# Optimization experiments

Measured on AMD Instinct MI355X. Metric: run time of the kernel, lower is better.

## Reference

```python
import jax, jax.numpy as jnp
import numpy as np
import math

N_HEAD = 16
N_LATENTS = 64
CHUNK = 128
ROPE_THETA = 10000.0


def _rope_cos_sin(T, D, theta):
    # D = head_dim; freqs over D/2 pairs
    inv = 1.0 / (theta ** (jnp.arange(0, D, 2, dtype=jnp.float32) / D))  # [D/2]
    ang = jnp.arange(T, dtype=jnp.float32)[:, None] * inv[None, :]       # [T, D/2]
    return jnp.cos(ang), jnp.sin(ang)


def _apply_rope(k, cos, sin):
    # k: [B, T, H, D]; pairs are consecutive (2i, 2i+1)
    B, T, H, D = k.shape
    kr = k.reshape(B, T, H, D // 2, 2)
    a, b = kr[..., 0], kr[..., 1]
    c = cos[None, :, None, :]
    s = sin[None, :, None, :]
    out = jnp.stack([a * c - b * s, a * s + b * c], axis=-1)
    return out.reshape(B, T, H, D).astype(k.dtype)


def setup_inputs() -> dict:
    key = jax.random.key(0)
    ks = jax.random.split(key, 6)
    B, T, C = 8, 4096, 1024
    H, L = N_HEAD, N_LATENTS
    D = C // H
    std_in = 1.0 / math.sqrt(C)
    return {
        "x": jax.random.normal(ks[0], (B, T, C), jnp.float32),
        "latent_queries": jax.random.normal(ks[1], (1, L, H, D), jnp.float32) * (1.0 / math.sqrt(D)),
        "W_k": jax.random.normal(ks[2], (C, C), jnp.float32) * std_in,
        "W_v": jax.random.normal(ks[3], (C, C), jnp.float32) * std_in,
        "W_g": jax.random.normal(ks[4], (H * L, C), jnp.float32) * std_in,
        "W_p": jax.random.normal(ks[5], (C, C), jnp.float32) * std_in,
    }


def reference(x, latent_queries, W_k, W_v, W_g, W_p):
    B, T, C = x.shape
    H, L, cs = N_HEAD, N_LATENTS, CHUNK
    D = C // H
    scale = 1.0 / math.sqrt(D)

    k = (x @ W_k.T).reshape(B, T, H, D)
    v = (x @ W_v.T).reshape(B, T, H, D)
    cos, sin = _rope_cos_sin(T, D, ROPE_THETA)
    k = _apply_rope(k, cos, sin)

    # softmax-gated latent mixing weights: [B, T, H, L]
    gates = jax.nn.softmax((x @ W_g.T).reshape(B, T, H, L) * scale, axis=-1)

    q = jnp.transpose(latent_queries, (0, 2, 1, 3))          # [1, H, L, D]
    nc = T // cs
    kc = jnp.transpose(k, (0, 2, 1, 3)).reshape(B, H, nc, cs, D)
    vc = jnp.transpose(v, (0, 2, 1, 3)).reshape(B, H, nc, cs, D)

    # per-chunk SDPA with torch is_causal semantics: top-left aligned
    # lower-triangular mask (latent row i attends chunk cols j <= i)
    scores = jnp.einsum('zhld,bhncd->bhnlc', q, kc) * scale   # [B,H,nc,L,cs]
    causal = jnp.arange(cs)[None, :] <= jnp.arange(L)[:, None]  # [L, cs]
    scores = jnp.where(causal[None, None, None], scores, -jnp.inf)
    probs = jax.nn.softmax(scores, axis=-1)
    # matmul with V per chunk, SUM over chunks (as in the torch loop)
    attn = jnp.einsum('bhnlc,bhncd->bhld', probs, vc)         # [B,H,L,D]

    # weighted combine: einsum('bhls,bhtl->bhts') then [B,T,C]
    weighted = jnp.einsum('bhld,bthl->bthd', attn, gates)
    out = weighted.reshape(B, T, C) @ W_p.T
    return out
```

## Files before the change

### kernel.cpp

```cpp
#include <hip/hip_runtime.h>
#include <hip/hip_bf16.h>

typedef unsigned short u16;
typedef __attribute__((ext_vector_type(8))) short bf16x8;
typedef __attribute__((ext_vector_type(4))) float f32x4;
typedef __attribute__((ext_vector_type(4))) unsigned short u16x4;

#define DEVI static __device__ __forceinline__

DEVI u16 f2bf(float f) {
    union { __hip_bfloat16 h; u16 u; } cv;
    cv.h = __float2bfloat16(f);
    return cv.u;
}
DEVI float bf2f(u16 u) {
    union { u16 u; __hip_bfloat16 h; } cv;
    cv.u = u;
    return __bfloat162float(cv.h);
}

DEVI void gload_lds16(const void* g, void* l) {
    __builtin_amdgcn_global_load_lds(
        (const __attribute__((address_space(1))) unsigned int*)g,
        (__attribute__((address_space(3))) unsigned int*)l, 16, 0, 0);
}

#define BAR asm volatile("s_barrier" ::: "memory")
#define VMW(N) asm volatile("s_waitcnt vmcnt(" #N ")" ::: "memory")

__global__ void k_cvt(const float* __restrict__ in, u16* __restrict__ out, int n4) {
    int i = blockIdx.x * blockDim.x + threadIdx.x;
    int stride = gridDim.x * blockDim.x;
    for (; i < n4; i += stride) {
        float4 v = ((const float4*)in)[i];
        u16x4 o;
        o.x = f2bf(v.x); o.y = f2bf(v.y); o.z = f2bf(v.z); o.w = f2bf(v.w);
        ((u16x4*)out)[i] = o;
    }
}

__global__ void k_rope(float2* __restrict__ tab) {
    int i = blockIdx.x * 256 + threadIdx.x;
    int t = i >> 5, j = i & 31;
    float inv = powf(10000.f, -(float)j / 32.f);
    float ang = (float)t * inv;
    float s, c;
    sincosf(ang, &s, &c);
    tab[i] = make_float2(c, s);
}

template<int MODE>
__global__ __launch_bounds__(512, 2) void k_gemm256(
    const u16* __restrict__ A, const u16* __restrict__ Bw,
    void* __restrict__ Cout, const float2* __restrict__ rope)
{
    extern __shared__ char lds[];
    const int tid = threadIdx.x;
    const int lane = tid & 63, wid = tid >> 6;
    const int wr = wid >> 2, wc = wid & 3;
    const int koff = (lane >> 4) * 16;

    const int GX = (MODE == 0) ? 8 : 4;
    const int kx = GX >> 1;
    int orig = blockIdx.x + blockIdx.y * GX;
    int xcd = orig & 7, i = orig >> 3;
    int bx = (xcd % kx) * 2 + (i & 1);
    int by = (xcd / kx) * 32 + (i >> 1);
    const int row0 = by * 256, col0 = bx * 256;

    auto stage = [&](int s) {
        const int t = s >> 2;
        const int isB = s & 1;
        const int kh = (s >> 1) & 1;
        char* base = lds + isB * 65536 + (t & 1) * 32768 + kh * 16384;
        const int kbase = t * 64 + kh * 32;
#pragma unroll
        for (int j = 0; j < 2; ++j) {
            int idx = j * 512 + tid;
            int r = idx >> 2;
            int kc = idx & 3;
            int grow;
            if (isB) {
                grow = col0 + r;
            } else {
                grow = row0 + r;
                if (MODE == 0)
                    grow = ((grow >> 11) << 12) | (((grow >> 6) & 31) << 7) | (grow & 63);
            }
            const u16* g = (isB ? Bw : A) + (size_t)grow * 1024 + kbase + kc * 8;
            gload_lds16(g, base + j * 8192 + wid * 1024);
        }
    };

    bf16x8 af[8];
    bf16x8 bq[2];
    f32x4 acc[8][4];
#pragma unroll
    for (int m = 0; m < 8; ++m)
#pragma unroll
        for (int n = 0; n < 4; ++n) acc[m][n] = f32x4{0.f, 0.f, 0.f, 0.f};

#define LDA(T, KH) do { \
    const char* ab_ = lds + ((T) & 1) * 32768 + (KH) * 16384; \
    _Pragma("unroll") \
    for (int mf = 0; mf < 8; ++mf) \
        af[mf] = *(const bf16x8*)(ab_ + (wr * 128 + mf * 16 + (lane & 15)) * 64 + koff); \
} while (0)

#define LDB(T, KH, NH) do { \
    const char* bb_ = lds + 65536 + ((T) & 1) * 32768 + (KH) * 16384; \
    bq[0] = *(const bf16x8*)(bb_ + (wc * 64 + ((NH) * 2)     * 16 + (lane & 15)) * 64 + koff); \
    bq[1] = *(const bf16x8*)(bb_ + (wc * 64 + ((NH) * 2 + 1) * 16 + (lane & 15)) * 64 + koff); \
} while (0)

#define MMA(NH) do { \
    __builtin_amdgcn_s_setprio(1); \
    _Pragma("unroll") \
    for (int mf = 0; mf < 8; ++mf) { \
        acc[mf][2 * (NH)]     = __builtin_amdgcn_mfma_f32_16x16x32_bf16(af[mf], bq[0], acc[mf][2 * (NH)], 0, 0, 0); \
        acc[mf][2 * (NH) + 1] = __builtin_amdgcn_mfma_f32_16x16x32_bf16(af[mf], bq[1], acc[mf][2 * (NH) + 1], 0, 0, 0); \
    } \
    __builtin_amdgcn_s_setprio(0); \
} while (0)

#pragma unroll 1
    for (int s = 0; s < 7; ++s) stage(s);
    VMW(10);
    BAR;

#pragma unroll 1
    for (int t = 0; t < 14; ++t) {
        LDA(t, 0); LDB(t, 0, 0);
        stage(4 * t + 7);
        BAR; MMA(0); BAR;
        LDB(t, 0, 1);
        stage(4 * t + 8);
        BAR; MMA(1); VMW(10); BAR;
        LDA(t, 1); LDB(t, 1, 0);
        stage(4 * t + 9);
        BAR; MMA(0); BAR;
        LDB(t, 1, 1);
        stage(4 * t + 10);
        BAR; MMA(1); VMW(10); BAR;
    }
    LDA(14, 0); LDB(14, 0, 0); stage(63); BAR; MMA(0); BAR;
    LDB(14, 0, 1);                         BAR; MMA(1); VMW(8); BAR;
    LDA(14, 1); LDB(14, 1, 0);             BAR; MMA(0); BAR;
    LDB(14, 1, 1);                         BAR; MMA(1); VMW(4); BAR;
    LDA(15, 0); LDB(15, 0, 0);             BAR; MMA(0); BAR;
    LDB(15, 0, 1);                         BAR; MMA(1); VMW(0); BAR;
    LDA(15, 1); LDB(15, 1, 0);             BAR; MMA(0); BAR;
    LDB(15, 1, 1);                         BAR; MMA(1);

#undef LDA
#undef LDB
#undef MMA

    const int rbase = row0 + wr * 128 + ((lane >> 4) << 2);
    const int cbase = col0 + wc * 64 + (lane & 15);
#pragma unroll
    for (int mf = 0; mf < 8; ++mf) {
#pragma unroll
        for (int nf = 0; nf < 4; ++nf) {
            const int gc = cbase + nf * 16;
#pragma unroll
            for (int r = 0; r < 4; ++r) {
                const int gr = rbase + mf * 16 + r;
                float v = acc[mf][nf][r];
                if (MODE == 0) {
                    float o = __shfl_xor(v, 1);
                    float res;
                    if (gc < 1024) {
                        int t = (((gr >> 6) & 31) << 7) | (gr & 63);
                        float2 cs = rope[t * 32 + ((gc & 63) >> 1)];
                        res = (gc & 1) ? (o * cs.y + v * cs.x) : (v * cs.x - o * cs.y);
                    } else {
                        res = v;
                    }
                    ((u16*)Cout)[(size_t)gr * 2048 + gc] = f2bf(res);
                } else if (MODE == 1) {
                    ((u16*)Cout)[(size_t)gr * 1024 + gc] = f2bf(v);
                } else {
                    ((float*)Cout)[(size_t)gr * 1024 + gc] = v;
                }
            }
        }
    }
}

__global__ __launch_bounds__(256, 2) void k_attn(
    const u16* __restrict__ kv, const float* __restrict__ lq, float* __restrict__ attnT)
{
    __shared__ char smem[65536];
    const int tid = threadIdx.x;
    const int lane = tid & 63, wid = tid >> 6;
    const int gidx = blockIdx.x & 3;
    const int bh = blockIdx.x >> 2;
    const int b = bh >> 4, h = bh & 15;

    bf16x8 qf[4][2];
#pragma unroll
    for (int lb = 0; lb < 4; ++lb)
#pragma unroll
        for (int kb = 0; kb < 2; ++kb) {
            const float* src = lq + ((size_t)(lb * 16 + (lane & 15)) * 16 + h) * 64 + kb * 32 + (lane >> 4) * 8;
            float4 v0 = ((const float4*)src)[0];
            float4 v1 = ((const float4*)src)[1];
            union { bf16x8 v; u16 u[8]; } pk;
            pk.u[0] = f2bf(v0.x * 0.125f); pk.u[1] = f2bf(v0.y * 0.125f);
            pk.u[2] = f2bf(v0.z * 0.125f); pk.u[3] = f2bf(v0.w * 0.125f);
            pk.u[4] = f2bf(v1.x * 0.125f); pk.u[5] = f2bf(v1.y * 0.125f);
            pk.u[6] = f2bf(v1.z * 0.125f); pk.u[7] = f2bf(v1.w * 0.125f);
            qf[lb][kb] = pk.v;
        }

    char* Pl = smem + wid * 16384;
    char* Vb = smem + wid * 16384 + 8192;
    u16* Vl = (u16*)Vb;

    f32x4 accT[4][4];
#pragma unroll
    for (int i = 0; i < 4; ++i)
#pragma unroll
        for (int j = 0; j < 4; ++j) accT[i][j] = f32x4{0.f, 0.f, 0.f, 0.f};

#pragma unroll 1
    for (int ci = 0; ci < 2; ++ci) {
        const int n = gidx * 8 + wid * 2 + ci;
        const size_t krow = (size_t)b * 2048 + (size_t)n * 64;

#pragma unroll
        for (int j = 0; j < 8; ++j) {
            const u16* g = kv + (krow + j * 8 + (lane >> 3)) * 2048 + 1024 + h * 64 + (lane & 7) * 8;
            gload_lds16(g, Vb + j * 1024);
        }

        f32x4 S[4][4];
#pragma unroll
        for (int i = 0; i < 4; ++i)
#pragma unroll
            for (int j = 0; j < 4; ++j) S[i][j] = f32x4{0.f, 0.f, 0.f, 0.f};
#pragma unroll
        for (int kb = 0; kb < 2; ++kb) {
            bf16x8 kf[4];
#pragma unroll
            for (int cb = 0; cb < 4; ++cb)
                kf[cb] = *(const bf16x8*)(kv + (krow + cb * 16 + (lane & 15)) * 2048 + h * 64 + kb * 32 + (lane >> 4) * 8);
#pragma unroll
            for (int lb = 0; lb < 4; ++lb)
#pragma unroll
                for (int cb = 0; cb < 4; ++cb)
                    S[lb][cb] = __builtin_amdgcn_mfma_f32_16x16x32_bf16(qf[lb][kb], kf[cb], S[lb][cb], 0, 0, 0);
        }

#pragma unroll
        for (int lb = 0; lb < 4; ++lb) {
#pragma unroll
            for (int r = 0; r < 4; ++r) {
                const int l = lb * 16 + (lane >> 4) * 4 + r;
                const int c0 = lane & 15;
                float vv[4];
                float m = -3e30f;
#pragma unroll
                for (int cb = 0; cb < 4; ++cb) {
                    int c = cb * 16 + c0;
                    vv[cb] = (c <= l) ? S[lb][cb][r] : -3e30f;
                    m = fmaxf(m, vv[cb]);
                }
                m = fmaxf(m, __shfl_xor(m, 1));
                m = fmaxf(m, __shfl_xor(m, 2));
                m = fmaxf(m, __shfl_xor(m, 4));
                m = fmaxf(m, __shfl_xor(m, 8));
                float p[4];
                float sum = 0.f;
#pragma unroll
                for (int cb = 0; cb < 4; ++cb) {
                    int c = cb * 16 + c0;
                    p[cb] = (c <= l) ? __expf(vv[cb] - m) : 0.f;
                    sum += p[cb];
                }
                sum += __shfl_xor(sum, 1);
                sum += __shfl_xor(sum, 2);
                sum += __shfl_xor(sum, 4);
                sum += __shfl_xor(sum, 8);
                const float inv = 1.f / sum;
#pragma unroll
                for (int cb = 0; cb < 4; ++cb) {
                    int c = cb * 16 + c0;
                    int byte = (l * 128 + c * 2) ^ ((l & 7) << 4);
                    *(u16*)(Pl + byte) = f2bf(p[cb] * inv);
                }
            }
        }

        asm volatile("s_waitcnt vmcnt(0)" ::: "memory");

#pragma unroll
        for (int kb = 0; kb < 2; ++kb) {
            bf16x8 pf[4];
#pragma unroll
            for (int lf = 0; lf < 4; ++lf) {
                int l = lf * 16 + (lane & 15);
                int byte = (l * 128 + (kb * 32 + (lane >> 4) * 8) * 2) ^ ((l & 7) << 4);
                pf[lf] = *(const bf16x8*)(Pl + byte);
            }
#pragma unroll
            for (int mf = 0; mf < 4; ++mf) {
                const int d = mf * 16 + (lane & 15);
                const int cb2 = kb * 32 + (lane >> 4) * 8;
                union { bf16x8 v; u16 u[8]; } vt;
#pragma unroll
                for (int e = 0; e < 8; ++e) vt.u[e] = Vl[(cb2 + e) * 64 + d];
#pragma unroll
                for (int lf = 0; lf < 4; ++lf)
                    accT[mf][lf] = __builtin_amdgcn_mfma_f32_16x16x32_bf16(vt.v, pf[lf], accT[mf][lf], 0, 0, 0);
            }
        }
    }

    float* red = (float*)smem;
#pragma unroll
    for (int mf = 0; mf < 4; ++mf)
#pragma unroll
        for (int lf = 0; lf < 4; ++lf)
#pragma unroll
            for (int r = 0; r < 4; ++r)
                red[wid * 4096 + (mf * 16 + (lane >> 4) * 4 + r) * 64 + lf * 16 + (lane & 15)] = accT[mf][lf][r];
    __syncthreads();
    for (int idx = tid; idx < 4096; idx += 256) {
        float s = red[idx] + red[4096 + idx] + red[8192 + idx] + red[12288 + idx];
        atomicAdd(&attnT[(size_t)bh * 4096 + idx], s);
    }
}

__global__ __launch_bounds__(256, 4) void k_weighted(
    const u16* __restrict__ logits, const float* __restrict__ attnT, u16* __restrict__ wout)
{
    const int tid = threadIdx.x, lane = tid & 63, wid = tid >> 6;
    const int bh = blockIdx.x >> 5, tt = blockIdx.x & 31;
    const int b = bh >> 4, h = bh & 15;
    const int t0 = tt * 128 + wid * 32;

    const float* at = attnT + (size_t)bh * 4096;
    bf16x8 bfr[4][2];
#pragma unroll
    for (int nf = 0; nf < 4; ++nf)
#pragma unroll
        for (int kb = 0; kb < 2; ++kb) {
            const float* src = at + (nf * 16 + (lane & 15)) * 64 + kb * 32 + (lane >> 4) * 8;
            float4 v0 = ((const float4*)src)[0];
            float4 v1 = ((const float4*)src)[1];
            union { bf16x8 v; u16 u[8]; } pk;
            pk.u[0] = f2bf(v0.x); pk.u[1] = f2bf(v0.y); pk.u[2] = f2bf(v0.z); pk.u[3] = f2bf(v0.w);
            pk.u[4] = f2bf(v1.x); pk.u[5] = f2bf(v1.y); pk.u[6] = f2bf(v1.z); pk.u[7] = f2bf(v1.w);
            bfr[nf][kb] = pk.v;
        }

    f32x4 acc[2][4];
#pragma unroll
    for (int i = 0; i < 2; ++i)
#pragma unroll
        for (int j = 0; j < 4; ++j) acc[i][j] = f32x4{0.f, 0.f, 0.f, 0.f};

#pragma unroll
    for (int mf = 0; mf < 2; ++mf) {
        const int t = t0 + mf * 16 + (lane & 15);
        const u16* lrow = logits + ((size_t)b * 4096 + t) * 1024 + h * 64 + (lane >> 4) * 8;
        bf16x8 l0 = *(const bf16x8*)lrow;
        bf16x8 l1 = *(const bf16x8*)(lrow + 32);
        float va[16];
#pragma unroll
        for (int j = 0; j < 8; ++j) {
            va[j] = bf2f((u16)l0[j]) * 0.125f;
            va[8 + j] = bf2f((u16)l1[j]) * 0.125f;
        }
        float m = va[0];
#pragma unroll
        for (int j = 1; j < 16; ++j) m = fmaxf(m, va[j]);
        m = fmaxf(m, __shfl_xor(m, 16));
        m = fmaxf(m, __shfl_xor(m, 32));
        float sum = 0.f;
#pragma unroll
        for (int j = 0; j < 16; ++j) { va[j] = __expf(va[j] - m); sum += va[j]; }
        sum += __shfl_xor(sum, 16);
        sum += __shfl_xor(sum, 32);
        const float inv = 1.f / sum;
        union { bf16x8 v; u16 u[8]; } a0, a1;
#pragma unroll
        for (int j = 0; j < 8; ++j) {
            a0.u[j] = f2bf(va[j] * inv);
            a1.u[j] = f2bf(va[8 + j] * inv);
        }
#pragma unroll
        for (int nf = 0; nf < 4; ++nf) {
            acc[mf][nf] = __builtin_amdgcn_mfma_f32_16x16x32_bf16(a0.v, bfr[nf][0], acc[mf][nf], 0, 0, 0);
            acc[mf][nf] = __builtin_amdgcn_mfma_f32_16x16x32_bf16(a1.v, bfr[nf][1], acc[mf][nf], 0, 0, 0);
        }
    }

#pragma unroll
    for (int mf = 0; mf < 2; ++mf)
#pragma unroll
        for (int nf = 0; nf < 4; ++nf)
#pragma unroll
            for (int r = 0; r < 4; ++r) {
                int t = t0 + mf * 16 + (lane >> 4) * 4 + r;
                wout[((size_t)b * 4096 + t) * 1024 + h * 64 + nf * 16 + (lane & 15)] = f2bf(acc[mf][nf][r]);
            }
}

extern "C" void kernel_launch(void* const* d_in, const int* in_sizes, int n_in,
                              void* d_out, int out_size, void* d_ws, size_t ws_size,
                              hipStream_t stream)
{
    const float* x  = (const float*)d_in[0];
    const float* lq = (const float*)d_in[1];
    const float* Wk = (const float*)d_in[2];
    const float* Wv = (const float*)d_in[3];
    const float* Wg = (const float*)d_in[4];
    const float* Wp = (const float*)d_in[5];

    char* ws = (char*)d_ws;
    u16*    wkv   = (u16*)(ws + 0);
    u16*    wg    = (u16*)(ws + 4194304);
    u16*    wp    = (u16*)(ws + 6291456);
    float2* rope  = (float2*)(ws + 8388608);
    float*  attnT = (float*)(ws + 9437184);
    u16*    kv    = (u16*)(ws + 11534336);
    u16* logits = (u16*)d_out;
    u16* xb     = (u16*)((char*)d_out + 67108864);

    hipFuncSetAttribute((const void*)k_gemm256<0>, hipFuncAttributeMaxDynamicSharedMemorySize, 131072);
    hipFuncSetAttribute((const void*)k_gemm256<1>, hipFuncAttributeMaxDynamicSharedMemorySize, 131072);
    hipFuncSetAttribute((const void*)k_gemm256<2>, hipFuncAttributeMaxDynamicSharedMemorySize, 131072);

    hipMemsetAsync(attnT, 0, 128 * 4096 * sizeof(float), stream);

    k_cvt<<<2048, 256, 0, stream>>>(x, xb, 33554432 / 4);
    k_cvt<<<512, 256, 0, stream>>>(Wk, wkv, 1048576 / 4);
    k_cvt<<<512, 256, 0, stream>>>(Wv, wkv + 1048576, 1048576 / 4);
    k_cvt<<<512, 256, 0, stream>>>(Wg, wg, 1048576 / 4);
    k_cvt<<<512, 256, 0, stream>>>(Wp, wp, 1048576 / 4);
    k_rope<<<512, 256, 0, stream>>>(rope);

    k_gemm256<0><<<dim3(8, 64), 512, 131072, stream>>>(xb, wkv, kv, rope);
    k_gemm256<1><<<dim3(4, 128), 512, 131072, stream>>>(xb, wg, logits, nullptr);
    k_attn<<<512, 256, 0, stream>>>(kv, lq, attnT);
    k_weighted<<<4096, 256, 0, stream>>>(logits, attnT, kv);
    k_gemm256<2><<<dim3(4, 128), 512, 131072, stream>>>(kv, wp, d_out, nullptr);
}
```

Measured before the change: 581.3 us.

## Swizzle LDS k-chunks to avoid bank conflicts and merge MMA phases

Applies an XOR swizzle to the 16-byte k-chunk position, both when staging global rows into LDS and when reading A/B fragments, so the fragment reads spread across LDS banks. The main loop is also restructured: all four B fragments are loaded at once and a single 32-MFMA block runs per k-half. This halves the barriers per iteration and stages two loads at a time with a shallower prefetch depth. In exchange it uses more registers for B fragments and changes the wait counts, which could hurt latency hiding.

```diff
diff --git a/kernel.cpp b/kernel.cpp
--- a/kernel.cpp
+++ b/kernel.cpp
@@ -58,7 +58,7 @@
     const int tid = threadIdx.x;
     const int lane = tid & 63, wid = tid >> 6;
     const int wr = wid >> 2, wc = wid & 3;
-    const int koff = (lane >> 4) * 16;
+    const int kswz = (((lane >> 4) ^ ((lane >> 1) & 3)) << 4);
 
     const int GX = (MODE == 0) ? 8 : 4;
     const int kx = GX >> 1;
@@ -87,13 +87,14 @@
                 if (MODE == 0)
                     grow = ((grow >> 11) << 12) | (((grow >> 6) & 31) << 7) | (grow & 63);
             }
-            const u16* g = (isB ? Bw : A) + (size_t)grow * 1024 + kbase + kc * 8;
+            const u16* g = (isB ? Bw : A) + (size_t)grow * 1024 + kbase
+                         + ((kc ^ ((idx >> 3) & 3)) * 8);
             gload_lds16(g, base + j * 8192 + wid * 1024);
         }
     };
 
     bf16x8 af[8];
-    bf16x8 bq[2];
+    bf16x8 bq[4];
     f32x4 acc[8][4];
 #pragma unroll
     for (int m = 0; m < 8; ++m)
@@ -104,57 +105,48 @@
     const char* ab_ = lds + ((T) & 1) * 32768 + (KH) * 16384; \
     _Pragma("unroll") \
     for (int mf = 0; mf < 8; ++mf) \
-        af[mf] = *(const bf16x8*)(ab_ + (wr * 128 + mf * 16 + (lane & 15)) * 64 + koff); \
+        af[mf] = *(const bf16x8*)(ab_ + (wr * 128 + mf * 16 + (lane & 15)) * 64 + kswz); \
 } while (0)
 
-#define LDB(T, KH, NH) do { \
+#define LDB(T, KH) do { \
     const char* bb_ = lds + 65536 + ((T) & 1) * 32768 + (KH) * 16384; \
-    bq[0] = *(const bf16x8*)(bb_ + (wc * 64 + ((NH) * 2)     * 16 + (lane & 15)) * 64 + koff); \
-    bq[1] = *(const bf16x8*)(bb_ + (wc * 64 + ((NH) * 2 + 1) * 16 + (lane & 15)) * 64 + koff); \
+    _Pragma("unroll") \
+    for (int nf = 0; nf < 4; ++nf) \
+        bq[nf] = *(const bf16x8*)(bb_ + (wc * 64 + nf * 16 + (lane & 15)) * 64 + kswz); \
 } while (0)
 
-#define MMA(NH) do { \
+#define MMAALL do { \
     __builtin_amdgcn_s_setprio(1); \
     _Pragma("unroll") \
-    for (int mf = 0; mf < 8; ++mf) { \
-        acc[mf][2 * (NH)]     = __builtin_amdgcn_mfma_f32_16x16x32_bf16(af[mf], bq[0], acc[mf][2 * (NH)], 0, 0, 0); \
-        acc[mf][2 * (NH) + 1] = __builtin_amdgcn_mfma_f32_16x16x32_bf16(af[mf], bq[1], acc[mf][2 * (NH) + 1], 0, 0, 0); \
-    } \
+    for (int mf = 0; mf < 8; ++mf) \
+        _Pragma("unroll") \
+        for (int nf = 0; nf < 4; ++nf) \
+            acc[mf][nf] = __builtin_amdgcn_mfma_f32_16x16x32_bf16(af[mf], bq[nf], acc[mf][nf], 0, 0, 0); \
     __builtin_amdgcn_s_setprio(0); \
 } while (0)
 
 #pragma unroll 1
-    for (int s = 0; s < 7; ++s) stage(s);
-    VMW(10);
+    for (int s = 0; s < 6; ++s) stage(s);
+    VMW(8);
     BAR;
 
 #pragma unroll 1
     for (int t = 0; t < 14; ++t) {
-        LDA(t, 0); LDB(t, 0, 0);
-        stage(4 * t + 7);
-        BAR; MMA(0); BAR;
-        LDB(t, 0, 1);
-        stage(4 * t + 8);
-        BAR; MMA(1); VMW(10); BAR;
-        LDA(t, 1); LDB(t, 1, 0);
-        stage(4 * t + 9);
-        BAR; MMA(0); BAR;
-        LDB(t, 1, 1);
-        stage(4 * t + 10);
-        BAR; MMA(1); VMW(10); BAR;
-    }
-    LDA(14, 0); LDB(14, 0, 0); stage(63); BAR; MMA(0); BAR;
-    LDB(14, 0, 1);                         BAR; MMA(1); VMW(8); BAR;
-    LDA(14, 1); LDB(14, 1, 0);             BAR; MMA(0); BAR;
-    LDB(14, 1, 1);                         BAR; MMA(1); VMW(4); BAR;
-    LDA(15, 0); LDB(15, 0, 0);             BAR; MMA(0); BAR;
-    LDB(15, 0, 1);                         BAR; MMA(1); VMW(0); BAR;
-    LDA(15, 1); LDB(15, 1, 0);             BAR; MMA(0); BAR;
-    LDB(15, 1, 1);                         BAR; MMA(1);
+        LDA(t, 0); LDB(t, 0);
+        stage(4 * t + 6); stage(4 * t + 7);
+        BAR; MMAALL; VMW(8); BAR;
+        LDA(t, 1); LDB(t, 1);
+        stage(4 * t + 8); stage(4 * t + 9);
+        BAR; MMAALL; VMW(8); BAR;
+    }
+    LDA(14, 0); LDB(14, 0); stage(62); stage(63); BAR; MMAALL; VMW(8); BAR;
+    LDA(14, 1); LDB(14, 1);                        BAR; MMAALL; VMW(4); BAR;
+    LDA(15, 0); LDB(15, 0);                        BAR; MMAALL; VMW(0); BAR;
+    LDA(15, 1); LDB(15, 1);                        BAR; MMAALL;
 
 #undef LDA
 #undef LDB
-#undef MMA
+#undef MMAALL
 
     const int rbase = row0 + wr * 128 + ((lane >> 4) << 2);
     const int cbase = col0 + wc * 64 + (lane & 15);
```

Measured after the change: 573.4 us. No clear change (-1.4%).
